# Kernel optimization log

Hardware: AMD Instinct MI355X
Metric: run time of the kernel (lower is better)

The kernel has to match this reference:

```python
import jax, jax.numpy as jnp
import numpy as np

B, U, D_DEC, D_ENC = 32, 4096, 512, 512
ATT_UNITS, NUM_HEADS = 512, 4
HEAD_DIM = ATT_UNITS // NUM_HEADS
CONV_FILTERS, CONV_K = 32, 31
INIT = 0.075


def setup_inputs() -> dict:
    key = jax.random.key(0)
    ks = jax.random.split(key, 12)
    u = lambda k, shape: jax.random.uniform(k, shape, jnp.float32, -INIT, INIT)
    return {
        "dec_state": jax.random.normal(ks[0], (B, D_DEC), jnp.float32),
        "enc_state": jax.random.normal(ks[1], (B, U, D_ENC), jnp.float32),
        "prev_attention_weights": jax.random.uniform(ks[2], (B, U), jnp.float32),
        # stacked per-head Dense params
        "Wphi": u(ks[3], (NUM_HEADS, D_DEC, HEAD_DIM)),
        "bphi": jnp.zeros((NUM_HEADS, HEAD_DIM), jnp.float32),
        "Wpsi": u(ks[4], (NUM_HEADS, D_ENC, HEAD_DIM)),
        "bpsi": jnp.zeros((NUM_HEADS, HEAD_DIM), jnp.float32),
        # Conv1D kernel in WIO layout: (kernel_size, in_ch=1, out_ch=32), no bias
        "conv_kernel": jax.random.uniform(ks[5], (CONV_K, 1, CONV_FILTERS), jnp.float32, -0.1, 0.1),
        "Wloc": u(ks[6], (CONV_FILTERS, NUM_HEADS)),
        "Wout": u(ks[7], (NUM_HEADS * D_ENC, ATT_UNITS)),
        "bout": jnp.zeros((ATT_UNITS,), jnp.float32),
    }


def reference(dec_state, enc_state, prev_attention_weights,
              Wphi, bphi, Wpsi, bpsi, conv_kernel, Wloc, Wout, bout):
    # location features: Conv1D(same, no bias) over prev attention weights
    loc_feat = jax.lax.conv_general_dilated(
        prev_attention_weights[:, :, None], conv_kernel,
        window_strides=(1,), padding="SAME",
        dimension_numbers=("NWC", "WIO", "NWC"))            # (B, U, 32)
    loc_bias = loc_feat @ Wloc                                 # (B, U, H)
    loc_bias = jnp.transpose(loc_bias, (0, 2, 1))              # (B, H, U)

    # batched per-head projections (replaces the Python per-head loop)
    phi_s = jnp.einsum("bd,hdk->bhk", dec_state, Wphi) + bphi          # (B, H, hd)
    psi_h = jnp.einsum("bue,hek->bhuk", enc_state, Wpsi) + bpsi[:, None, :]  # (B, H, U, hd)

    energy = jnp.einsum("bhk,bhuk->bhu", phi_s, psi_h) + loc_bias      # (B, H, U)
    attn = jax.nn.softmax(energy, axis=-1)                              # (B, H, U)

    context = jnp.einsum("bhu,bue->bhe", attn, enc_state)               # (B, H, E)
    combined = context.reshape(context.shape[0], -1)                    # (B, H*E)
    context_vector = combined @ Wout + bout                             # (B, ATT_UNITS)
    attention_weights = jnp.mean(attn, axis=1)                          # (B, U)
    return context_vector, attention_weights
```

## Files before the change

### kernel.cpp

```cpp
#include <hip/hip_runtime.h>
#include <math.h>

#define B  32
#define U  4096
#define D  512
#define H  4
#define HD 128
#define CK 31
#define CF 32
#define AU 512

#define BPB    32
#define ROWS_W 32

#define LOG2E 1.4426950408889634f

static __device__ __forceinline__ float readlane_f(float v, int l) {
    return __int_as_float(__builtin_amdgcn_readlane(__float_as_int(v), l));
}
static __device__ __forceinline__ float fast_exp2(float x) {
    return __builtin_amdgcn_exp2f(x);
}

__global__ __launch_bounds__(256) void prep_kernel(
    const float* __restrict__ dec,
    const float* __restrict__ Wphi,
    const float* __restrict__ bphi,
    const float* __restrict__ Wpsi,
    const float* __restrict__ bpsi,
    const float* __restrict__ convk,
    const float* __restrict__ Wloc,
    float* __restrict__ ws_v,
    float* __restrict__ ws_const,
    float* __restrict__ ws_ck)
{
    __shared__ float decs[D];
    __shared__ float phis2[2][HD];
    __shared__ float phis[HD];
    const int b = blockIdx.x / H, h = blockIdx.x % H;
    const int tid = threadIdx.x;

    for (int i = tid; i < D; i += 256) decs[i] = dec[b * D + i];
    __syncthreads();

    {
        const int k = tid & 127, half = tid >> 7;
        const int d0 = half * 256;
        float acc = 0.f;
        const float* wp = Wphi + (size_t)h * D * HD + (size_t)d0 * HD + k;
        #pragma unroll 8
        for (int d = 0; d < 256; ++d) acc += decs[d0 + d] * wp[(size_t)d * HD];
        phis2[half][k] = acc;
    }
    __syncthreads();
    if (tid < HD) phis[tid] = phis2[0][tid] + phis2[1][tid] + bphi[h * HD + tid];
    __syncthreads();

    if (tid == 0) {
        float c = 0.f;
        for (int k = 0; k < HD; ++k) c += phis[k] * bpsi[h * HD + k];
        ws_const[b * H + h] = c * LOG2E;
    }

    for (int e = tid; e < D; e += 256) {
        const float* wq = Wpsi + ((size_t)h * D + e) * HD;
        float acc = 0.f;
        #pragma unroll 8
        for (int k = 0; k < HD; ++k) acc += wq[k] * phis[k];
        ws_v[((size_t)b * H + h) * D + e] = acc * LOG2E;
    }

    if (blockIdx.x == 0 && tid < CK * H) {
        int t = tid / H, hh = tid % H;
        float acc = 0.f;
        for (int f = 0; f < CF; ++f) acc += convk[t * CF + f] * Wloc[f * H + hh];
        ws_ck[t * H + hh] = acc * LOG2E;
    }
}

__global__ __launch_bounds__(256, 4) void fused_pass1(
    const float* __restrict__ enc,
    const float* __restrict__ prevw,
    const float* __restrict__ ws_v,
    const float* __restrict__ ws_const,
    const float* __restrict__ ws_ck,
    float* __restrict__ energy,
    float* __restrict__ pctx,
    float* __restrict__ pms)
{
    const int b    = blockIdx.y;
    const int blk  = blockIdx.x;
    const int tid  = threadIdx.x;
    const int lane = tid & 63;
    const int wave = tid >> 6;
    const int ubase = (blk * 4 + wave) * ROWS_W;

    __shared__ float lctx[4][H][D];
    __shared__ float lms[4][H][2];
    __shared__ float lalpha[H][4];

    float4 v0[H], v1[H];
    #pragma unroll
    for (int h = 0; h < H; ++h) {
        const float* vp = ws_v + ((size_t)b * H + h) * D;
        v0[h] = *(const float4*)(vp + lane * 4);
        v1[h] = *(const float4*)(vp + 256 + lane * 4);
    }
    float ckr[H] = {0.f, 0.f, 0.f, 0.f};
    if (lane < CK) {
        #pragma unroll
        for (int h = 0; h < H; ++h) ckr[h] = ws_ck[lane * H + h];
    }
    float ct[H];
    #pragma unroll
    for (int h = 0; h < H; ++h) ct[h] = ws_const[b * H + h];

    float w0;
    {
        const int gi = ubase - 15 + lane;
        w0 = (gi >= 0 && gi < U) ? prevw[b * U + gi] : 0.f;
    }

    float m0 = -3.402823466e38f, m1 = m0, m2 = m0, m3 = m0;
    float s0 = 0.f, s1 = 0.f, s2 = 0.f, s3 = 0.f;
    float4 z = {0.f, 0.f, 0.f, 0.f};
    float4 c00 = z, c01 = z, c10 = z, c11 = z, c20 = z, c21 = z, c30 = z, c31 = z;

    const bool b16 = (lane & 16) != 0;
    const bool b32 = (lane & 32) != 0;

    const float* encb = enc + ((size_t)b * U + ubase) * D;
    float4 e0 = *(const float4*)(encb + lane * 4);
    float4 e1 = *(const float4*)(encb + 256 + lane * 4);

    for (int r = 0; r < ROWS_W; ++r) {
        float4 n0, n1;
        if (r < ROWS_W - 1) {
            const float* nx = encb + (size_t)(r + 1) * D;
            n0 = *(const float4*)(nx + lane * 4);
            n1 = *(const float4*)(nx + 256 + lane * 4);
        }
        const int u = ubase + r;
        float pw = __int_as_float(
            __builtin_amdgcn_ds_bpermute((r + lane) << 2, __float_as_int(w0)));

        float p0 = pw * ckr[0]
            + e0.x*v0[0].x + e0.y*v0[0].y + e0.z*v0[0].z + e0.w*v0[0].w
            + e1.x*v1[0].x + e1.y*v1[0].y + e1.z*v1[0].z + e1.w*v1[0].w;
        float p1 = pw * ckr[1]
            + e0.x*v0[1].x + e0.y*v0[1].y + e0.z*v0[1].z + e0.w*v0[1].w
            + e1.x*v1[1].x + e1.y*v1[1].y + e1.z*v1[1].z + e1.w*v1[1].w;
        float p2 = pw * ckr[2]
            + e0.x*v0[2].x + e0.y*v0[2].y + e0.z*v0[2].z + e0.w*v0[2].w
            + e1.x*v1[2].x + e1.y*v1[2].y + e1.z*v1[2].z + e1.w*v1[2].w;
        float p3 = pw * ckr[3]
            + e0.x*v0[3].x + e0.y*v0[3].y + e0.z*v0[3].z + e0.w*v0[3].w
            + e1.x*v1[3].x + e1.y*v1[3].y + e1.z*v1[3].z + e1.w*v1[3].w;

        float keepA = b16 ? p1 : p0, sendA = b16 ? p0 : p1;
        float a  = keepA + __shfl_xor(sendA, 16);
        float keepB = b16 ? p3 : p2, sendB = b16 ? p2 : p3;
        float bb = keepB + __shfl_xor(sendB, 16);
        float keepC = b32 ? bb : a, sendC = b32 ? a : bb;
        float c = keepC + __shfl_xor(sendC, 32);
        c += __shfl_xor(c, 1);
        c += __shfl_xor(c, 2);
        c += __shfl_xor(c, 4);
        c += __shfl_xor(c, 8);
        float eh0 = readlane_f(c, 0)  + ct[0];
        float eh1 = readlane_f(c, 16) + ct[1];
        float eh2 = readlane_f(c, 32) + ct[2];
        float eh3 = readlane_f(c, 48) + ct[3];

        if (lane < H) {
            float ev = (lane == 0) ? eh0 : (lane == 1) ? eh1 : (lane == 2) ? eh2 : eh3;
            energy[((size_t)b * H + lane) * U + u] = ev;
        }

        float mn0 = fmaxf(m0, eh0), mn1 = fmaxf(m1, eh1);
        float mn2 = fmaxf(m2, eh2), mn3 = fmaxf(m3, eh3);
        if (mn0 > m0 || mn1 > m1 || mn2 > m2 || mn3 > m3) {
            float a0 = fast_exp2(m0 - mn0), a1 = fast_exp2(m1 - mn1);
            float a2 = fast_exp2(m2 - mn2), a3 = fast_exp2(m3 - mn3);
            s0 *= a0; s1 *= a1; s2 *= a2; s3 *= a3;
            c00.x*=a0; c00.y*=a0; c00.z*=a0; c00.w*=a0; c01.x*=a0; c01.y*=a0; c01.z*=a0; c01.w*=a0;
            c10.x*=a1; c10.y*=a1; c10.z*=a1; c10.w*=a1; c11.x*=a1; c11.y*=a1; c11.z*=a1; c11.w*=a1;
            c20.x*=a2; c20.y*=a2; c20.z*=a2; c20.w*=a2; c21.x*=a2; c21.y*=a2; c21.z*=a2; c21.w*=a2;
            c30.x*=a3; c30.y*=a3; c30.z*=a3; c30.w*=a3; c31.x*=a3; c31.y*=a3; c31.z*=a3; c31.w*=a3;
            m0 = mn0; m1 = mn1; m2 = mn2; m3 = mn3;
        }
        float w0e = fast_exp2(eh0 - m0), w1e = fast_exp2(eh1 - m1);
        float w2e = fast_exp2(eh2 - m2), w3e = fast_exp2(eh3 - m3);
        s0 += w0e; s1 += w1e; s2 += w2e; s3 += w3e;
        c00.x += w0e*e0.x; c00.y += w0e*e0.y; c00.z += w0e*e0.z; c00.w += w0e*e0.w;
        c01.x += w0e*e1.x; c01.y += w0e*e1.y; c01.z += w0e*e1.z; c01.w += w0e*e1.w;
        c10.x += w1e*e0.x; c10.y += w1e*e0.y; c10.z += w1e*e0.z; c10.w += w1e*e0.w;
        c11.x += w1e*e1.x; c11.y += w1e*e1.y; c11.z += w1e*e1.z; c11.w += w1e*e1.w;
        c20.x += w2e*e0.x; c20.y += w2e*e0.y; c20.z += w2e*e0.z; c20.w += w2e*e0.w;
        c21.x += w2e*e1.x; c21.y += w2e*e1.y; c21.z += w2e*e1.z; c21.w += w2e*e1.w;
        c30.x += w3e*e0.x; c30.y += w3e*e0.y; c30.z += w3e*e0.z; c30.w += w3e*e0.w;
        c31.x += w3e*e1.x; c31.y += w3e*e1.y; c31.z += w3e*e1.z; c31.w += w3e*e1.w;

        e0 = n0; e1 = n1;
    }

    *(float4*)&lctx[wave][0][lane * 4]       = c00;
    *(float4*)&lctx[wave][0][256 + lane * 4] = c01;
    *(float4*)&lctx[wave][1][lane * 4]       = c10;
    *(float4*)&lctx[wave][1][256 + lane * 4] = c11;
    *(float4*)&lctx[wave][2][lane * 4]       = c20;
    *(float4*)&lctx[wave][2][256 + lane * 4] = c21;
    *(float4*)&lctx[wave][3][lane * 4]       = c30;
    *(float4*)&lctx[wave][3][256 + lane * 4] = c31;
    if (lane == 0) {
        lms[wave][0][0] = m0; lms[wave][0][1] = s0;
        lms[wave][1][0] = m1; lms[wave][1][1] = s1;
        lms[wave][2][0] = m2; lms[wave][2][1] = s2;
        lms[wave][3][0] = m3; lms[wave][3][1] = s3;
    }
    __syncthreads();

    const size_t pbase = ((size_t)(b * BPB + blk)) * H;
    if (tid < H) {
        const int h = tid;
        float M = fmaxf(fmaxf(lms[0][h][0], lms[1][h][0]),
                        fmaxf(lms[2][h][0], lms[3][h][0]));
        float S = 0.f;
        #pragma unroll
        for (int w = 0; w < 4; ++w) {
            float al = fast_exp2(lms[w][h][0] - M);
            lalpha[h][w] = al;
            S += al * lms[w][h][1];
        }
        pms[(pbase + h) * 2]     = M;
        pms[(pbase + h) * 2 + 1] = S;
    }
    __syncthreads();

    #pragma unroll
    for (int h = 0; h < H; ++h) {
        const float a0 = lalpha[h][0], a1 = lalpha[h][1];
        const float a2 = lalpha[h][2], a3 = lalpha[h][3];
        #pragma unroll
        for (int half = 0; half < 2; ++half) {
            const int d = tid + half * 256;
            float val = a0 * lctx[0][h][d] + a1 * lctx[1][h][d]
                      + a2 * lctx[2][h][d] + a3 * lctx[3][h][d];
            pctx[(pbase + h) * D + d] = val;
        }
    }
}

__global__ __launch_bounds__(256) void combine_outproj_kernel(
    const float* __restrict__ pctx,
    const float* __restrict__ pms,
    const float* __restrict__ Wout,
    const float* __restrict__ bout,
    float* __restrict__ outv,
    float* __restrict__ MS)
{
    const int bh = blockIdx.x;
    const int b = bh >> 2, h = bh & 3;
    const int tid = threadIdx.x;
    __shared__ float sm[BPB], ss[BPB], salpha[BPB];
    __shared__ float MSsh[2];
    __shared__ float c_s[D];

    if (tid < BPB) {
        sm[tid] = pms[(((size_t)b * BPB + tid) * H + h) * 2];
        ss[tid] = pms[(((size_t)b * BPB + tid) * H + h) * 2 + 1];
    }
    __syncthreads();
    if (tid == 0) {
        float M = -3.402823466e38f;
        for (int i = 0; i < BPB; ++i) M = fmaxf(M, sm[i]);
        float S = 0.f;
        for (int i = 0; i < BPB; ++i) {
            float al = fast_exp2(sm[i] - M);
            salpha[i] = al;
            S += al * ss[i];
        }
        MSsh[0] = M; MSsh[1] = S;
        MS[bh * 2] = M; MS[bh * 2 + 1] = S;
    }
    __syncthreads();
    const float invS = 1.0f / MSsh[1];

    float acc0 = 0.f, acc1 = 0.f;
    const float* base = pctx + ((size_t)b * BPB * H + h) * D;
    #pragma unroll 4
    for (int i = 0; i < BPB; ++i) {
        float al = salpha[i];
        const float* p = base + (size_t)i * H * D;
        acc0 += al * p[tid];
        acc1 += al * p[tid + 256];
    }
    c_s[tid]       = acc0 * invS;
    c_s[tid + 256] = acc1 * invS;
    __syncthreads();

    float a0 = (h == 0) ? bout[tid]       : 0.f;
    float a1 = (h == 0) ? bout[tid + 256] : 0.f;
    const float* W = Wout + (size_t)h * D * AU;
    #pragma unroll 8
    for (int i = 0; i < D; ++i) {
        const float ci = c_s[i];
        a0 += ci * W[(size_t)i * AU + tid];
        a1 += ci * W[(size_t)i * AU + tid + 256];
    }
    atomicAdd(&outv[(size_t)b * AU + tid],       a0);
    atomicAdd(&outv[(size_t)b * AU + tid + 256], a1);
}

__global__ __launch_bounds__(256) void attw_kernel(
    const float* __restrict__ energy,
    const float* __restrict__ MS,
    float* __restrict__ attw)
{
    const int b = blockIdx.x;
    const int u = blockIdx.y * 256 + threadIdx.x;
    float acc = 0.f;
    #pragma unroll
    for (int h = 0; h < H; ++h) {
        const float M  = MS[(b * H + h) * 2];
        const float iS = 1.0f / MS[(b * H + h) * 2 + 1];
        acc += fast_exp2(energy[((size_t)b * H + h) * U + u] - M) * iS;
    }
    attw[(size_t)b * U + u] = acc * 0.25f;
}

extern "C" void kernel_launch(void* const* d_in, const int* in_sizes, int n_in,
                              void* d_out, int out_size, void* d_ws, size_t ws_size,
                              hipStream_t stream) {
    const float* dec   = (const float*)d_in[0];
    const float* enc   = (const float*)d_in[1];
    const float* prevw = (const float*)d_in[2];
    const float* Wphi  = (const float*)d_in[3];
    const float* bphi  = (const float*)d_in[4];
    const float* Wpsi  = (const float*)d_in[5];
    const float* bpsi  = (const float*)d_in[6];
    const float* convk = (const float*)d_in[7];
    const float* Wloc  = (const float*)d_in[8];
    const float* Wout  = (const float*)d_in[9];
    const float* bout  = (const float*)d_in[10];

    float* out  = (float*)d_out;
    float* outv = out;
    float* attw = out + B * AU;

    float* ws        = (float*)d_ws;
    float* ws_v      = ws;
    float* ws_const  = ws + 65536;
    float* ws_ck     = ws + 65664;
    float* ws_energy = ws + 65792;
    float* ws_pctx   = ws_energy + (size_t)B*H*U;
    float* ws_pms    = ws_pctx + (size_t)B*BPB*H*D;
    float* ws_MS     = ws_pms + (size_t)B*BPB*H*2;

    hipMemsetAsync(outv, 0, (size_t)B * AU * sizeof(float), stream);

    prep_kernel<<<dim3(B * H), 256, 0, stream>>>(dec, Wphi, bphi, Wpsi, bpsi,
                                                 convk, Wloc, ws_v, ws_const, ws_ck);
    fused_pass1<<<dim3(BPB, B), 256, 0, stream>>>(enc, prevw, ws_v, ws_const,
                                                  ws_ck, ws_energy, ws_pctx, ws_pms);
    combine_outproj_kernel<<<dim3(B * H), 256, 0, stream>>>(ws_pctx, ws_pms, Wout,
                                                            bout, outv, ws_MS);
    attw_kernel<<<dim3(B, U / 256), 256, 0, stream>>>(ws_energy, ws_MS, attw);
}
```

Measured before the change: 451.9 us.

## Deepen enc prefetch to two rows and split output projection into parallel tail kernel

The main pass now prefetches encoder rows two iterations ahead instead of one, to hide more global-load latency, at the cost of extra registers. The output projection moves out of the combine kernel, which only writes the normalized context. It now runs in a new tail kernel alongside the attention-weight computation, with the K dimension split into 256-wide chunks across 16 extra blocks per batch and accumulated via atomics. This raises the parallelism of the projection from 128 blocks and removes one kernel's serialized work, but adds a workspace round trip for the context.

```diff
diff --git a/kernel.cpp b/kernel.cpp
--- a/kernel.cpp
+++ b/kernel.cpp
@@ -132,13 +132,15 @@
     const float* encb = enc + ((size_t)b * U + ubase) * D;
     float4 e0 = *(const float4*)(encb + lane * 4);
     float4 e1 = *(const float4*)(encb + 256 + lane * 4);
+    float4 n0 = *(const float4*)(encb + D + lane * 4);
+    float4 n1 = *(const float4*)(encb + D + 256 + lane * 4);
 
     for (int r = 0; r < ROWS_W; ++r) {
-        float4 n0, n1;
-        if (r < ROWS_W - 1) {
-            const float* nx = encb + (size_t)(r + 1) * D;
-            n0 = *(const float4*)(nx + lane * 4);
-            n1 = *(const float4*)(nx + 256 + lane * 4);
+        float4 q0, q1;
+        if (r < ROWS_W - 2) {
+            const float* nx = encb + (size_t)(r + 2) * D;
+            q0 = *(const float4*)(nx + lane * 4);
+            q1 = *(const float4*)(nx + 256 + lane * 4);
         }
         const int u = ubase + r;
         float pw = __int_as_float(
@@ -201,7 +203,7 @@
         c30.x += w3e*e0.x; c30.y += w3e*e0.y; c30.z += w3e*e0.z; c30.w += w3e*e0.w;
         c31.x += w3e*e1.x; c31.y += w3e*e1.y; c31.z += w3e*e1.z; c31.w += w3e*e1.w;
 
-        e0 = n0; e1 = n1;
+        e0 = n0; e1 = n1; n0 = q0; n1 = q1;
     }
 
     *(float4*)&lctx[wave][0][lane * 4]       = c00;
@@ -251,12 +253,10 @@
     }
 }
 
-__global__ __launch_bounds__(256) void combine_outproj_kernel(
+__global__ __launch_bounds__(256) void combine_kernel(
     const float* __restrict__ pctx,
     const float* __restrict__ pms,
-    const float* __restrict__ Wout,
-    const float* __restrict__ bout,
-    float* __restrict__ outv,
+    float* __restrict__ ctx,
     float* __restrict__ MS)
 {
     const int bh = blockIdx.x;
@@ -264,7 +264,6 @@
     const int tid = threadIdx.x;
     __shared__ float sm[BPB], ss[BPB], salpha[BPB];
     __shared__ float MSsh[2];
-    __shared__ float c_s[D];
 
     if (tid < BPB) {
         sm[tid] = pms[(((size_t)b * BPB + tid) * H + h) * 2];
@@ -295,38 +294,49 @@
         acc0 += al * p[tid];
         acc1 += al * p[tid + 256];
     }
-    c_s[tid]       = acc0 * invS;
-    c_s[tid + 256] = acc1 * invS;
-    __syncthreads();
-
-    float a0 = (h == 0) ? bout[tid]       : 0.f;
-    float a1 = (h == 0) ? bout[tid + 256] : 0.f;
-    const float* W = Wout + (size_t)h * D * AU;
-    #pragma unroll 8
-    for (int i = 0; i < D; ++i) {
-        const float ci = c_s[i];
-        a0 += ci * W[(size_t)i * AU + tid];
-        a1 += ci * W[(size_t)i * AU + tid + 256];
-    }
-    atomicAdd(&outv[(size_t)b * AU + tid],       a0);
-    atomicAdd(&outv[(size_t)b * AU + tid + 256], a1);
-}
-
-__global__ __launch_bounds__(256) void attw_kernel(
+    ctx[(size_t)bh * D + tid]       = acc0 * invS;
+    ctx[(size_t)bh * D + tid + 256] = acc1 * invS;
+}
+
+__global__ __launch_bounds__(256) void tail_kernel(
     const float* __restrict__ energy,
     const float* __restrict__ MS,
-    float* __restrict__ attw)
+    const float* __restrict__ ctx,
+    const float* __restrict__ Wout,
+    const float* __restrict__ bout,
+    float* __restrict__ attw,
+    float* __restrict__ outv)
 {
     const int b = blockIdx.x;
-    const int u = blockIdx.y * 256 + threadIdx.x;
-    float acc = 0.f;
-    #pragma unroll
-    for (int h = 0; h < H; ++h) {
-        const float M  = MS[(b * H + h) * 2];
-        const float iS = 1.0f / MS[(b * H + h) * 2 + 1];
-        acc += fast_exp2(energy[((size_t)b * H + h) * U + u] - M) * iS;
-    }
-    attw[(size_t)b * U + u] = acc * 0.25f;
+    const int role = blockIdx.y;
+    const int tid = threadIdx.x;
+
+    if (role < 16) {
+        const int u = role * 256 + tid;
+        float acc = 0.f;
+        #pragma unroll
+        for (int h = 0; h < H; ++h) {
+            const float M  = MS[(b * H + h) * 2];
+            const float iS = 1.0f / MS[(b * H + h) * 2 + 1];
+            acc += fast_exp2(energy[((size_t)b * H + h) * U + u] - M) * iS;
+        }
+        attw[(size_t)b * U + u] = acc * 0.25f;
+    } else {
+        const int idx = role - 16;
+        const int jh  = idx & 1;
+        const int kc  = idx >> 1;
+        const int j   = jh * 256 + tid;
+        const int i0  = kc * 256;
+        __shared__ float c_s[256];
+        c_s[tid] = ctx[(size_t)b * (H * D) + i0 + tid];
+        __syncthreads();
+
+        float acc = (kc == 0) ? bout[j] : 0.f;
+        #pragma unroll 8
+        for (int i = 0; i < 256; ++i)
+            acc += c_s[i] * Wout[(size_t)(i0 + i) * AU + j];
+        atomicAdd(&outv[(size_t)b * AU + j], acc);
+    }
 }
 
 extern "C" void kernel_launch(void* const* d_in, const int* in_sizes, int n_in,
@@ -356,6 +366,7 @@
     float* ws_pctx   = ws_energy + (size_t)B*H*U;
     float* ws_pms    = ws_pctx + (size_t)B*BPB*H*D;
     float* ws_MS     = ws_pms + (size_t)B*BPB*H*2;
+    float* ws_ctx    = ws_MS + 256;
 
     hipMemsetAsync(outv, 0, (size_t)B * AU * sizeof(float), stream);
 
@@ -363,7 +374,7 @@
                                                  convk, Wloc, ws_v, ws_const, ws_ck);
     fused_pass1<<<dim3(BPB, B), 256, 0, stream>>>(enc, prevw, ws_v, ws_const,
                                                   ws_ck, ws_energy, ws_pctx, ws_pms);
-    combine_outproj_kernel<<<dim3(B * H), 256, 0, stream>>>(ws_pctx, ws_pms, Wout,
-                                                            bout, outv, ws_MS);
-    attw_kernel<<<dim3(B, U / 256), 256, 0, stream>>>(ws_energy, ws_MS, attw);
-}
+    combine_kernel<<<dim3(B * H), 256, 0, stream>>>(ws_pctx, ws_pms, ws_ctx, ws_MS);
+    tail_kernel<<<dim3(B, 32), 256, 0, stream>>>(ws_energy, ws_MS, ws_ctx,
+                                                 Wout, bout, attw, outv);
+}
```

Result: faster. 435.6 us (-3.6%).
